# Optimization experiments

Hardware: AMD Instinct MI355X
Metric: run time of the kernel (lower is better)

## Reference

```python
import jax, jax.numpy as jnp
import numpy as np

B, S, DIM = 4, 1024, 2048
HQ, HKV, HD = 16, 4, 128  # query heads, kv heads, head dim
G = HQ // HKV             # GQA group size


def _rope(t, freqs):
    # t: (B, S, H, HD); freqs: (S, HD//2) angles. Llama-style: adjacent pairs
    # (even, odd) treated as (real, imag) and rotated by exp(i*theta).
    tr = t.reshape(t.shape[:-1] + (HD // 2, 2))
    cos = jnp.cos(freqs)[None, :, None, :]
    sin = jnp.sin(freqs)[None, :, None, :]
    re = tr[..., 0] * cos - tr[..., 1] * sin
    im = tr[..., 0] * sin + tr[..., 1] * cos
    return jnp.stack([re, im], axis=-1).reshape(t.shape)


def setup_inputs() -> dict:
    key = jax.random.key(0)
    ks = jax.random.split(key, 5)
    x = jax.random.normal(ks[0], (B, S, DIM), jnp.float32)
    # rotary angles: outer(t, 1/10000^(2i/d))
    inv_freq = 1.0 / (10000.0 ** (np.arange(0, HD, 2, dtype=np.float32) / HD))
    freqs = jnp.asarray(np.outer(np.arange(S, dtype=np.float32), inv_freq))
    # additive causal mask (finite large negative for numerical safety)
    i = jnp.arange(S)
    mask = jnp.where(i[None, :] <= i[:, None], 0.0, -1e9).astype(jnp.float32)
    std = 0.02
    wq = jax.random.normal(ks[1], (HQ * HD, DIM), jnp.float32) * std
    wk = jax.random.normal(ks[2], (HKV * HD, DIM), jnp.float32) * std
    wv = jax.random.normal(ks[3], (HKV * HD, DIM), jnp.float32) * std
    wo = jax.random.normal(ks[4], (DIM, DIM), jnp.float32) * std
    return {"x": x, "start_pos": 0, "freqs": freqs, "mask": mask,
            "wq": wq, "wk": wk, "wv": wv, "wo": wo}


def reference(x, start_pos, freqs, mask, wq, wk, wv, wo):
    b, s, _ = x.shape
    q = (x @ wq.T).reshape(b, s, HQ, HD)
    k = (x @ wk.T).reshape(b, s, HKV, HD)
    v = (x @ wv.T).reshape(b, s, HKV, HD)
    q = _rope(q, freqs)
    k = _rope(k, freqs)
    # GQA: group query heads per kv head, avoiding repeat_kv materialization
    qg = q.reshape(b, s, HKV, G, HD)
    scores = jnp.einsum('bskgd,btkd->bkgst', qg, k) / np.float32(np.sqrt(HD))
    scores = scores + mask  # (S,S) broadcasts over (b, kv, g, s, t)
    p = jax.nn.softmax(scores, axis=-1)
    o = jnp.einsum('bkgst,btkd->bskgd', p, v).reshape(b, s, HQ * HD)
    return o @ wo.T
```

## Files before the change

kernel.cpp:

```cpp
#include <hip/hip_runtime.h>

typedef unsigned short u16;
typedef unsigned int u32;
typedef __bf16 bf16x8 __attribute__((ext_vector_type(8)));
typedef float floatx4 __attribute__((ext_vector_type(4)));

#if __has_builtin(__builtin_amdgcn_exp2f)
#define EXP2F(x) __builtin_amdgcn_exp2f(x)
#else
#define EXP2F(x) __expf((x) * 0.6931471805599453f)
#endif

__device__ __forceinline__ u16 f2bf(float x) {
  union { float f; u32 u; } v; v.f = x;
  u32 r = v.u + 0x7fffu + ((v.u >> 16) & 1u);
  return (u16)(r >> 16);
}
__device__ __forceinline__ float bf2f(u16 x) {
  union { float f; u32 u; } v; v.u = ((u32)x) << 16;
  return v.f;
}

__device__ __forceinline__ void gl_lds16(const u16* g, u16* l) {
  __builtin_amdgcn_global_load_lds((const __attribute__((address_space(1))) void*)g,
                                   (__attribute__((address_space(3))) void*)l, 16, 0, 0);
}

__global__ __launch_bounds__(256) void cvt_all(const float* __restrict__ x,
                                               const float* __restrict__ wq,
                                               const float* __restrict__ wk,
                                               const float* __restrict__ wv,
                                               const float* __restrict__ wo,
                                               u16* __restrict__ xb, u16* __restrict__ wqb,
                                               u16* __restrict__ wkb, u16* __restrict__ wvb,
                                               u16* __restrict__ wob) {
  int i = blockIdx.x * 256 + threadIdx.x;
  const float* s; u16* d; int off;
  if (i < 2097152)      { s = x;  d = xb;  off = 0; }
  else if (i < 3145728) { s = wq; d = wqb; off = 2097152; }
  else if (i < 3407872) { s = wk; d = wkb; off = 3145728; }
  else if (i < 3670016) { s = wv; d = wvb; off = 3407872; }
  else                  { s = wo; d = wob; off = 3670016; }
  i -= off;
  float4 v = ((const float4*)s)[i];
  uint2 o;
  o.x = (u32)f2bf(v.x) | ((u32)f2bf(v.y) << 16);
  o.y = (u32)f2bf(v.z) | ((u32)f2bf(v.w) << 16);
  ((uint2*)d)[i] = o;
}

__global__ __launch_bounds__(256) void rope_both(u16* __restrict__ qb, u16* __restrict__ kb,
                                                 const float* __restrict__ fr) {
  int idx = blockIdx.x * 256 + threadIdx.x;
  u16* t; int lgH; float scale;
  if (idx < 4194304) { t = qb; lgH = 4; scale = 0.08838834764831845f * 1.4426950408889634f; }
  else               { t = kb; lgH = 2; scale = 1.0f; idx -= 4194304; }
  int p = idx & 63;
  int bsh = idx >> 6;
  int s = (bsh >> lgH) & 1023;
  float th = fr[s * 64 + p];
  float sn, cs;
  sincosf(th, &sn, &cs);
  u32* base = (u32*)(t + (size_t)bsh * 128 + p * 2);
  u32 pr = *base;
  float e = bf2f((u16)(pr & 0xffffu));
  float o = bf2f((u16)(pr >> 16));
  u16 re = f2bf((e * cs - o * sn) * scale);
  u16 im = f2bf((e * sn + o * cs) * scale);
  *base = (u32)re | ((u32)im << 16);
}

__device__ __forceinline__ void gemm_core(const u16* __restrict__ A, const u16* __restrict__ Bw,
                                          u16* sA, u16* sB, int m0, int n0,
                                          floatx4 acc[4][4]) {
  const int tid = threadIdx.x;
  const int wave = tid >> 6, lane = tid & 63;
  const int quad = lane >> 4, l16 = lane & 15;
  const int wm = (wave >> 1) * 64, wn = (wave & 1) * 64;
  const int srow = wave * 8 + (lane >> 3);
  const int scol = (((lane & 7) ^ ((lane >> 3) & 7)) * 8);
  const int lds_off = wave * 512 + lane * 8;
  const int swA = (l16 & 7);
  for (int k0 = 0; k0 < 2048; k0 += 64) {
    __syncthreads();
    #pragma unroll
    for (int c = 0; c < 4; c++) {
      gl_lds16(A + (size_t)(m0 + c * 32 + srow) * 2048 + k0 + scol, sA + c * 2048 + lds_off);
      gl_lds16(Bw + (size_t)(n0 + c * 32 + srow) * 2048 + k0 + scol, sB + c * 2048 + lds_off);
    }
    __syncthreads();
    #pragma unroll
    for (int ks = 0; ks < 64; ks += 32) {
      const int pc = ((((ks >> 3) + quad) ^ swA) << 3);
      bf16x8 af[4], bw[4];
      #pragma unroll
      for (int i = 0; i < 4; i++)
        af[i] = *(const bf16x8*)&sA[(wm + i * 16 + l16) * 64 + pc];
      #pragma unroll
      for (int j = 0; j < 4; j++)
        bw[j] = *(const bf16x8*)&sB[(wn + j * 16 + l16) * 64 + pc];
      #pragma unroll
      for (int i = 0; i < 4; i++)
        #pragma unroll
        for (int j = 0; j < 4; j++)
          acc[i][j] = __builtin_amdgcn_mfma_f32_16x16x32_bf16(af[i], bw[j], acc[i][j], 0, 0, 0);
    }
  }
}

__global__ __launch_bounds__(256, 3) void gemm_qkv(const u16* __restrict__ xb,
                                                   const u16* __restrict__ wqb,
                                                   const u16* __restrict__ wkb,
                                                   const u16* __restrict__ wvb,
                                                   u16* __restrict__ qb, u16* __restrict__ kb,
                                                   u16* __restrict__ vtb) {
  __shared__ __align__(16) u16 sA[128 * 64];
  __shared__ __align__(16) u16 sB[128 * 64];
  const int by = blockIdx.y;
  const u16* Bw; int n0, mode;
  if (by < 16)      { Bw = wqb; n0 = by * 128;        mode = 0; }
  else if (by < 20) { Bw = wkb; n0 = (by - 16) * 128; mode = 1; }
  else              { Bw = wvb; n0 = (by - 20) * 128; mode = 2; }
  const int m0 = blockIdx.x * 128;
  floatx4 acc[4][4] = {};
  gemm_core(xb, Bw, sA, sB, m0, n0, acc);
  const int tid = threadIdx.x;
  const int wave = tid >> 6, lane = tid & 63;
  const int quad = lane >> 4, l16 = lane & 15;
  const int wm = (wave >> 1) * 64, wn = (wave & 1) * 64;
  #pragma unroll
  for (int i = 0; i < 4; i++) {
    #pragma unroll
    for (int j = 0; j < 4; j++) {
      const int row0 = m0 + wm + i * 16 + quad * 4;
      const int col = n0 + wn + j * 16 + l16;
      #pragma unroll
      for (int r = 0; r < 4; r++) {
        int m = row0 + r;
        u16 val = f2bf(acc[i][j][r]);
        if (mode == 0) {
          qb[(size_t)m * 2048 + col] = val;
        } else if (mode == 1) {
          kb[(size_t)m * 512 + col] = val;
        } else {
          int b = m >> 10, sI = m & 1023, kvh = col >> 7, hd = col & 127;
          vtb[((size_t)((b * 4 + kvh) * 128 + hd)) * 1024 + sI] = val;
        }
      }
    }
  }
}

__global__ __launch_bounds__(256, 3) void gemm_out(const u16* __restrict__ ob,
                                                   const u16* __restrict__ wob,
                                                   float* __restrict__ Cf) {
  __shared__ __align__(16) u16 sA[128 * 64];
  __shared__ __align__(16) u16 sB[128 * 64];
  const int m0 = blockIdx.x * 128, n0 = blockIdx.y * 128;
  floatx4 acc[4][4] = {};
  gemm_core(ob, wob, sA, sB, m0, n0, acc);
  const int tid = threadIdx.x;
  const int wave = tid >> 6, lane = tid & 63;
  const int quad = lane >> 4, l16 = lane & 15;
  const int wm = (wave >> 1) * 64, wn = (wave & 1) * 64;
  #pragma unroll
  for (int i = 0; i < 4; i++) {
    #pragma unroll
    for (int j = 0; j < 4; j++) {
      const int row0 = m0 + wm + i * 16 + quad * 4;
      const int col = n0 + wn + j * 16 + l16;
      #pragma unroll
      for (int r = 0; r < 4; r++)
        Cf[(size_t)(row0 + r) * 2048 + col] = acc[i][j][r];
    }
  }
}

__device__ __forceinline__ void attn_chunk(const u16* __restrict__ qbaseHead,
                                           const u16* __restrict__ kbase,
                                           const u16* __restrict__ vbase,
                                           int qr0, int kt_begin, int kt_end,
                                           u16* myP, floatx4 (&o_acc)[2][8],
                                           float (&l_part)[2], int quad, int l16) {
  const floatx4 vzero = {0.f, 0.f, 0.f, 0.f};
  #pragma unroll
  for (int i = 0; i < 2; i++) {
    l_part[i] = 0.f;
    #pragma unroll
    for (int j = 0; j < 8; j++) o_acc[i][j] = vzero;
  }
  bf16x8 aq[2][4];
  #pragma unroll
  for (int i = 0; i < 2; i++)
    #pragma unroll
    for (int ks = 0; ks < 4; ks++)
      aq[i][ks] = *(const bf16x8*)(qbaseHead + (size_t)(qr0 + i * 16 + l16) * 2048 + ks * 32 + quad * 8);

  bf16x8 bk[2][4];
  #pragma unroll
  for (int j = 0; j < 4; j++)
    bk[0][j] = *(const bf16x8*)(kbase + (size_t)(kt_begin * 64 + j * 16 + l16) * 512 + quad * 8);

  for (int kt = kt_begin; kt < kt_end; kt++) {
    const int t0 = kt * 64;
    const int t0n = (kt + 1 < kt_end) ? t0 + 64 : t0;
    floatx4 s_acc[4][2];
    #pragma unroll
    for (int j = 0; j < 4; j++)
      #pragma unroll
      for (int i = 0; i < 2; i++) s_acc[j][i] = vzero;
    bf16x8 bv[2][8];
    #pragma unroll
    for (int j2 = 0; j2 < 8; j2++)
      bv[0][j2] = *(const bf16x8*)(vbase + (size_t)(j2 * 16 + l16) * 1024 + t0 + quad * 8);
    #pragma unroll
    for (int ks = 0; ks < 4; ks++) {
      const int nks = (ks + 1) & 3;
      const int nt0 = (ks == 3) ? t0n : t0;
      #pragma unroll
      for (int j = 0; j < 4; j++)
        bk[(ks + 1) & 1][j] =
            *(const bf16x8*)(kbase + (size_t)(nt0 + j * 16 + l16) * 512 + nks * 32 + quad * 8);
      #pragma unroll
      for (int j = 0; j < 4; j++)
        #pragma unroll
        for (int i = 0; i < 2; i++)
          s_acc[j][i] = __builtin_amdgcn_mfma_f32_16x16x32_bf16(bk[ks & 1][j], aq[i][ks], s_acc[j][i], 0, 0, 0);
    }
    #pragma unroll
    for (int j2 = 0; j2 < 8; j2++)
      bv[1][j2] = *(const bf16x8*)(vbase + (size_t)(j2 * 16 + l16) * 1024 + t0 + 32 + quad * 8);
    const bool nomask = (t0 + 63 <= qr0);
    #pragma unroll
    for (int i = 0; i < 2; i++) {
      const int qrow = qr0 + i * 16 + l16;
      #pragma unroll
      for (int j = 0; j < 4; j++) {
        const int key0 = t0 + j * 16 + quad * 4;
        float e0, e1, e2, e3;
        if (nomask) {
          e0 = EXP2F(s_acc[j][i][0]);
          e1 = EXP2F(s_acc[j][i][1]);
          e2 = EXP2F(s_acc[j][i][2]);
          e3 = EXP2F(s_acc[j][i][3]);
        } else {
          e0 = (key0 + 0 <= qrow) ? EXP2F(s_acc[j][i][0]) : 0.f;
          e1 = (key0 + 1 <= qrow) ? EXP2F(s_acc[j][i][1]) : 0.f;
          e2 = (key0 + 2 <= qrow) ? EXP2F(s_acc[j][i][2]) : 0.f;
          e3 = (key0 + 3 <= qrow) ? EXP2F(s_acc[j][i][3]) : 0.f;
        }
        l_part[i] += (e0 + e1) + (e2 + e3);
        uint2 w;
        w.x = (u32)f2bf(e0) | ((u32)f2bf(e1) << 16);
        w.y = (u32)f2bf(e2) | ((u32)f2bf(e3) << 16);
        *(uint2*)&myP[(i * 16 + l16) * 68 + j * 16 + quad * 4] = w;
      }
    }
    #pragma unroll
    for (int ks2 = 0; ks2 < 2; ks2++) {
      bf16x8 ap[2];
      #pragma unroll
      for (int i = 0; i < 2; i++)
        ap[i] = *(const bf16x8*)&myP[(i * 16 + l16) * 68 + ks2 * 32 + quad * 8];
      #pragma unroll
      for (int i = 0; i < 2; i++)
        #pragma unroll
        for (int j2 = 0; j2 < 8; j2++)
          o_acc[i][j2] = __builtin_amdgcn_mfma_f32_16x16x32_bf16(ap[i], bv[ks2][j2], o_acc[i][j2], 0, 0, 0);
    }
  }
}

__device__ __forceinline__ void store_out(u16* __restrict__ obaseHead, int qr0,
                                          floatx4 (&o_acc)[2][8], float (&l_part)[2],
                                          int quad, int l16) {
  #pragma unroll
  for (int i = 0; i < 2; i++) {
    float lr = l_part[i];
    lr += __shfl_xor(lr, 16);
    lr += __shfl_xor(lr, 32);
    #pragma unroll
    for (int r = 0; r < 4; r++) {
      const float inv = 1.f / __shfl(lr, quad * 4 + r);
      const int row = qr0 + i * 16 + quad * 4 + r;
      #pragma unroll
      for (int j = 0; j < 8; j++)
        obaseHead[(size_t)row * 2048 + j * 16 + l16] = f2bf(o_acc[i][j][r] * inv);
    }
  }
}

__global__ __launch_bounds__(128)
__attribute__((amdgpu_waves_per_eu(2, 2)))
void flash_attn(const u16* __restrict__ q,
                const u16* __restrict__ k,
                const u16* __restrict__ vt,
                u16* __restrict__ o) {
  __shared__ __align__(16) char smem[26112];
  const int tid = threadIdx.x;
  const int wave = tid >> 6, lane = tid & 63;
  const int quad = lane >> 4, l16 = lane & 15;
  const int bi = blockIdx.x;
  const int h = bi & 63;
  const int b = h >> 4, hq = h & 15, kv = (hq >> 2);
  const int c = 31 - (bi >> 6);
  const int Tc = (32 * c + 31) / 64 + 1;
  const int tMid = Tc >> 1;
  u16* myP = (u16*)(smem + wave * 4352);
  float* ldsO = (float*)(smem + 8704);
  float* ldsL = (float*)(smem + 8704 + 16896);

  const u16* qbaseHead = q + (size_t)b * 2097152 + hq * 128;
  const u16* kbase = k + (size_t)b * 524288 + kv * 128;
  const u16* vbase = vt + (size_t)(b * 4 + kv) * 131072;
  u16* obaseHead = o + (size_t)b * 2097152 + hq * 128;

  floatx4 o_acc[2][8];
  float l_part[2];
  if (wave == 0) {
    attn_chunk(qbaseHead, kbase, vbase, c * 32, 0, tMid, myP, o_acc, l_part, quad, l16);
    #pragma unroll
    for (int i = 0; i < 2; i++) {
      ldsL[i * 64 + lane] = l_part[i];
      #pragma unroll
      for (int j = 0; j < 8; j++)
        #pragma unroll
        for (int r = 0; r < 4; r++)
          ldsO[(i * 16 + quad * 4 + r) * 132 + j * 16 + l16] = o_acc[i][j][r];
    }
    __syncthreads();
  } else {
    attn_chunk(qbaseHead, kbase, vbase, c * 32, tMid, Tc, myP, o_acc, l_part, quad, l16);
    __syncthreads();
    #pragma unroll
    for (int i = 0; i < 2; i++) {
      l_part[i] += ldsL[i * 64 + lane];
      #pragma unroll
      for (int j = 0; j < 8; j++)
        #pragma unroll
        for (int r = 0; r < 4; r++)
          o_acc[i][j][r] += ldsO[(i * 16 + quad * 4 + r) * 132 + j * 16 + l16];
    }
    store_out(obaseHead, c * 32, o_acc, l_part, quad, l16);
  }
}

extern "C" void kernel_launch(void* const* d_in, const int* in_sizes, int n_in,
                              void* d_out, int out_size, void* d_ws, size_t ws_size,
                              hipStream_t stream) {
  const float* x  = (const float*)d_in[0];
  const float* fr = (const float*)d_in[2];
  const float* wq = (const float*)d_in[4];
  const float* wk = (const float*)d_in[5];
  const float* wv = (const float*)d_in[6];
  const float* wo = (const float*)d_in[7];
  float* out = (float*)d_out;

  char* ws = (char*)d_ws;
  u16* xb  = (u16*)(ws + 0);
  u16* wqb = (u16*)(ws + 16777216);
  u16* wkb = (u16*)(ws + 25165824);
  u16* wvb = (u16*)(ws + 27262976);
  u16* wob = (u16*)(ws + 29360128);
  u16* qb  = (u16*)(ws + 37748736);
  u16* kb  = (u16*)(ws + 54525952);
  u16* vtb = (u16*)(ws + 58720256);
  u16* ob  = (u16*)(ws + 62914560);

  cvt_all<<<18432, 256, 0, stream>>>(x, wq, wk, wv, wo, xb, wqb, wkb, wvb, wob);
  gemm_qkv<<<dim3(32, 24), 256, 0, stream>>>(xb, wqb, wkb, wvb, qb, kb, vtb);
  rope_both<<<20480, 256, 0, stream>>>(qb, kb, fr);
  flash_attn<<<2048, 128, 0, stream>>>(qb, kb, vtb, ob);
  gemm_out<<<dim3(32, 16), 256, 0, stream>>>(ob, wob, out);
}
```

Baseline: 306.9 us.

## Share K/V tiles across GQA heads via swizzled LDS staging in flash attention

Restructures flash attention so each 256-thread block serves two query heads of one KV head over 64 query rows. K tiles (double-buffered) and V tiles are staged into LDS with async global-to-LDS loads and an XOR swizzle, so the four waves reuse one copy instead of each wave loading K/V from global memory. It drops the old split-KV two-wave reduction in favour of a causal-balanced block ordering (pairing short and long rows). The cost is two block-wide barriers per tile and fewer, larger blocks, which may lower occupancy.

```diff
diff --git a/kernel.cpp b/kernel.cpp
--- a/kernel.cpp
+++ b/kernel.cpp
@@ -176,12 +176,60 @@
   }
 }
 
-__device__ __forceinline__ void attn_chunk(const u16* __restrict__ qbaseHead,
-                                           const u16* __restrict__ kbase,
-                                           const u16* __restrict__ vbase,
-                                           int qr0, int kt_begin, int kt_end,
-                                           u16* myP, floatx4 (&o_acc)[2][8],
-                                           float (&l_part)[2], int quad, int l16) {
+__device__ __forceinline__ void store_out(u16* __restrict__ obaseHead, int qr0,
+                                          floatx4 (&o_acc)[2][8], float (&l_part)[2],
+                                          int quad, int l16) {
+  #pragma unroll
+  for (int i = 0; i < 2; i++) {
+    float lr = l_part[i];
+    lr += __shfl_xor(lr, 16);
+    lr += __shfl_xor(lr, 32);
+    #pragma unroll
+    for (int r = 0; r < 4; r++) {
+      const float inv = 1.f / __shfl(lr, quad * 4 + r);
+      const int row = qr0 + i * 16 + quad * 4 + r;
+      #pragma unroll
+      for (int j = 0; j < 8; j++)
+        obaseHead[(size_t)row * 2048 + j * 16 + l16] = f2bf(o_acc[i][j][r] * inv);
+    }
+  }
+}
+
+__global__ __launch_bounds__(256)
+__attribute__((amdgpu_waves_per_eu(2, 2)))
+void flash_attn(const u16* __restrict__ q,
+                const u16* __restrict__ k,
+                const u16* __restrict__ vt,
+                u16* __restrict__ o) {
+  __shared__ __align__(16) u16 sK[2][64 * 128];
+  __shared__ __align__(16) u16 sV[128 * 64];
+  __shared__ __align__(16) u16 sP[4][32 * 64];
+  const int tid = threadIdx.x;
+  const int wave = tid >> 6, lane = tid & 63;
+  const int quad = lane >> 4, l16 = lane & 15;
+  const int bi = blockIdx.x;
+  const int bkv = bi & 15;
+  const int b = bkv >> 2, kv = bkv & 3;
+  const int hp = (bi >> 4) & 1;
+  const int u = bi >> 5;
+  const int m = (u < 8) ? u : 23 - u;
+  const int qh = kv * 4 + hp * 2 + (wave >> 1);
+  const int qr0 = m * 64 + (wave & 1) * 32;
+
+  const u16* qbase = q + (size_t)b * 2097152 + qh * 128;
+  const u16* vbase = vt + (size_t)(b * 4 + kv) * 131072;
+  u16* obase = o + (size_t)b * 2097152 + qh * 128;
+  u16* myP = &sP[wave][0];
+
+  bf16x8 aq[2][4];
+  #pragma unroll
+  for (int i = 0; i < 2; i++)
+    #pragma unroll
+    for (int ks = 0; ks < 4; ks++)
+      aq[i][ks] = *(const bf16x8*)(qbase + (size_t)(qr0 + i * 16 + l16) * 2048 + ks * 32 + quad * 8);
+
+  floatx4 o_acc[2][8];
+  float l_part[2];
   const floatx4 vzero = {0.f, 0.f, 0.f, 0.f};
   #pragma unroll
   for (int i = 0; i < 2; i++) {
@@ -189,54 +237,71 @@
     #pragma unroll
     for (int j = 0; j < 8; j++) o_acc[i][j] = vzero;
   }
-  bf16x8 aq[2][4];
-  #pragma unroll
-  for (int i = 0; i < 2; i++)
-    #pragma unroll
-    for (int ks = 0; ks < 4; ks++)
-      aq[i][ks] = *(const bf16x8*)(qbaseHead + (size_t)(qr0 + i * 16 + l16) * 2048 + ks * 32 + quad * 8);
-
-  bf16x8 bk[2][4];
-  #pragma unroll
-  for (int j = 0; j < 4; j++)
-    bk[0][j] = *(const bf16x8*)(kbase + (size_t)(kt_begin * 64 + j * 16 + l16) * 512 + quad * 8);
-
-  for (int kt = kt_begin; kt < kt_end; kt++) {
-    const int t0 = kt * 64;
-    const int t0n = (kt + 1 < kt_end) ? t0 + 64 : t0;
+
+  #define STAGE_K(T, PAR)                                                         \
+    {                                                                             \
+      const u16* kb_t = k + (size_t)(b * 1024 + (T) * 64) * 512 + kv * 128;       \
+      _Pragma("unroll")                                                           \
+      for (int v = 0; v < 4; v++) {                                               \
+        int ci = v * 256 + tid;                                                   \
+        int r = ci >> 4, c = ci & 15;                                             \
+        gl_lds16(kb_t + r * 512 + ((c ^ (r & 7)) << 3), &sK[PAR][ci * 8]);        \
+      }                                                                           \
+    }
+  #define STAGE_V(T)                                                              \
+    {                                                                             \
+      _Pragma("unroll")                                                           \
+      for (int v = 0; v < 4; v++) {                                               \
+        int ci = v * 256 + tid;                                                   \
+        int r = ci >> 3, c = ci & 7;                                              \
+        gl_lds16(vbase + r * 1024 + (T) * 64 + ((c ^ (r & 7)) << 3), &sV[ci * 8]); \
+      }                                                                           \
+    }
+
+  STAGE_K(0, 0);
+  __syncthreads();
+
+  for (int t = 0; t <= m; t++) {
+    STAGE_V(t);
+    if (t < m) STAGE_K(t + 1, (t + 1) & 1);
+
+    const u16* kcur = &sK[t & 1][0];
     floatx4 s_acc[4][2];
     #pragma unroll
     for (int j = 0; j < 4; j++)
       #pragma unroll
       for (int i = 0; i < 2; i++) s_acc[j][i] = vzero;
-    bf16x8 bv[2][8];
-    #pragma unroll
-    for (int j2 = 0; j2 < 8; j2++)
-      bv[0][j2] = *(const bf16x8*)(vbase + (size_t)(j2 * 16 + l16) * 1024 + t0 + quad * 8);
+    bf16x8 bkA[4], bkB[4];
+    #pragma unroll
+    for (int j = 0; j < 4; j++) {
+      const int R = j * 16 + l16;
+      bkA[j] = *(const bf16x8*)&kcur[R * 128 + ((quad ^ (R & 7)) << 3)];
+    }
     #pragma unroll
     for (int ks = 0; ks < 4; ks++) {
-      const int nks = (ks + 1) & 3;
-      const int nt0 = (ks == 3) ? t0n : t0;
-      #pragma unroll
-      for (int j = 0; j < 4; j++)
-        bk[(ks + 1) & 1][j] =
-            *(const bf16x8*)(kbase + (size_t)(nt0 + j * 16 + l16) * 512 + nks * 32 + quad * 8);
+      bf16x8* cur = (ks & 1) ? bkB : bkA;
+      bf16x8* nxt = (ks & 1) ? bkA : bkB;
+      if (ks < 3) {
+        #pragma unroll
+        for (int j = 0; j < 4; j++) {
+          const int R = j * 16 + l16;
+          nxt[j] = *(const bf16x8*)&kcur[R * 128 + ((((ks + 1) * 4 + quad) ^ (R & 7)) << 3)];
+        }
+      }
       #pragma unroll
       for (int j = 0; j < 4; j++)
         #pragma unroll
         for (int i = 0; i < 2; i++)
-          s_acc[j][i] = __builtin_amdgcn_mfma_f32_16x16x32_bf16(bk[ks & 1][j], aq[i][ks], s_acc[j][i], 0, 0, 0);
-    }
-    #pragma unroll
-    for (int j2 = 0; j2 < 8; j2++)
-      bv[1][j2] = *(const bf16x8*)(vbase + (size_t)(j2 * 16 + l16) * 1024 + t0 + 32 + quad * 8);
-    const bool nomask = (t0 + 63 <= qr0);
+          s_acc[j][i] = __builtin_amdgcn_mfma_f32_16x16x32_bf16(cur[j], aq[i][ks], s_acc[j][i], 0, 0, 0);
+    }
+
+    const bool nomask = (t < m);
     #pragma unroll
     for (int i = 0; i < 2; i++) {
       const int qrow = qr0 + i * 16 + l16;
       #pragma unroll
       for (int j = 0; j < 4; j++) {
-        const int key0 = t0 + j * 16 + quad * 4;
+        const int key0 = t * 64 + j * 16 + quad * 4;
         float e0, e1, e2, e3;
         if (nomask) {
           e0 = EXP2F(s_acc[j][i][0]);
@@ -253,96 +318,39 @@
         uint2 w;
         w.x = (u32)f2bf(e0) | ((u32)f2bf(e1) << 16);
         w.y = (u32)f2bf(e2) | ((u32)f2bf(e3) << 16);
-        *(uint2*)&myP[(i * 16 + l16) * 68 + j * 16 + quad * 4] = w;
-      }
-    }
+        const int ri = i * 16 + l16;
+        *(uint2*)&myP[ri * 64 + (((2 * j + (quad >> 1)) ^ (ri & 7)) << 3) + (quad & 1) * 4] = w;
+      }
+    }
+
+    __syncthreads();
+
     #pragma unroll
     for (int ks2 = 0; ks2 < 2; ks2++) {
-      bf16x8 ap[2];
-      #pragma unroll
-      for (int i = 0; i < 2; i++)
-        ap[i] = *(const bf16x8*)&myP[(i * 16 + l16) * 68 + ks2 * 32 + quad * 8];
+      bf16x8 ap[2], bvf[8];
+      #pragma unroll
+      for (int j2 = 0; j2 < 8; j2++) {
+        const int R = j2 * 16 + l16;
+        bvf[j2] = *(const bf16x8*)&sV[R * 64 + (((ks2 * 4 + quad) ^ (R & 7)) << 3)];
+      }
+      #pragma unroll
+      for (int i = 0; i < 2; i++) {
+        const int ri = i * 16 + l16;
+        ap[i] = *(const bf16x8*)&myP[ri * 64 + (((ks2 * 4 + quad) ^ (ri & 7)) << 3)];
+      }
       #pragma unroll
       for (int i = 0; i < 2; i++)
         #pragma unroll
         for (int j2 = 0; j2 < 8; j2++)
-          o_acc[i][j2] = __builtin_amdgcn_mfma_f32_16x16x32_bf16(ap[i], bv[ks2][j2], o_acc[i][j2], 0, 0, 0);
-    }
-  }
-}
-
-__device__ __forceinline__ void store_out(u16* __restrict__ obaseHead, int qr0,
-                                          floatx4 (&o_acc)[2][8], float (&l_part)[2],
-                                          int quad, int l16) {
-  #pragma unroll
-  for (int i = 0; i < 2; i++) {
-    float lr = l_part[i];
-    lr += __shfl_xor(lr, 16);
-    lr += __shfl_xor(lr, 32);
-    #pragma unroll
-    for (int r = 0; r < 4; r++) {
-      const float inv = 1.f / __shfl(lr, quad * 4 + r);
-      const int row = qr0 + i * 16 + quad * 4 + r;
-      #pragma unroll
-      for (int j = 0; j < 8; j++)
-        obaseHead[(size_t)row * 2048 + j * 16 + l16] = f2bf(o_acc[i][j][r] * inv);
-    }
-  }
-}
-
-__global__ __launch_bounds__(128)
-__attribute__((amdgpu_waves_per_eu(2, 2)))
-void flash_attn(const u16* __restrict__ q,
-                const u16* __restrict__ k,
-                const u16* __restrict__ vt,
-                u16* __restrict__ o) {
-  __shared__ __align__(16) char smem[26112];
-  const int tid = threadIdx.x;
-  const int wave = tid >> 6, lane = tid & 63;
-  const int quad = lane >> 4, l16 = lane & 15;
-  const int bi = blockIdx.x;
-  const int h = bi & 63;
-  const int b = h >> 4, hq = h & 15, kv = (hq >> 2);
-  const int c = 31 - (bi >> 6);
-  const int Tc = (32 * c + 31) / 64 + 1;
-  const int tMid = Tc >> 1;
-  u16* myP = (u16*)(smem + wave * 4352);
-  float* ldsO = (float*)(smem + 8704);
-  float* ldsL = (float*)(smem + 8704 + 16896);
-
-  const u16* qbaseHead = q + (size_t)b * 2097152 + hq * 128;
-  const u16* kbase = k + (size_t)b * 524288 + kv * 128;
-  const u16* vbase = vt + (size_t)(b * 4 + kv) * 131072;
-  u16* obaseHead = o + (size_t)b * 2097152 + hq * 128;
-
-  floatx4 o_acc[2][8];
-  float l_part[2];
-  if (wave == 0) {
-    attn_chunk(qbaseHead, kbase, vbase, c * 32, 0, tMid, myP, o_acc, l_part, quad, l16);
-    #pragma unroll
-    for (int i = 0; i < 2; i++) {
-      ldsL[i * 64 + lane] = l_part[i];
-      #pragma unroll
-      for (int j = 0; j < 8; j++)
-        #pragma unroll
-        for (int r = 0; r < 4; r++)
-          ldsO[(i * 16 + quad * 4 + r) * 132 + j * 16 + l16] = o_acc[i][j][r];
-    }
+          o_acc[i][j2] = __builtin_amdgcn_mfma_f32_16x16x32_bf16(ap[i], bvf[j2], o_acc[i][j2], 0, 0, 0);
+    }
+
     __syncthreads();
-  } else {
-    attn_chunk(qbaseHead, kbase, vbase, c * 32, tMid, Tc, myP, o_acc, l_part, quad, l16);
-    __syncthreads();
-    #pragma unroll
-    for (int i = 0; i < 2; i++) {
-      l_part[i] += ldsL[i * 64 + lane];
-      #pragma unroll
-      for (int j = 0; j < 8; j++)
-        #pragma unroll
-        for (int r = 0; r < 4; r++)
-          o_acc[i][j][r] += ldsO[(i * 16 + quad * 4 + r) * 132 + j * 16 + l16];
-    }
-    store_out(obaseHead, c * 32, o_acc, l_part, quad, l16);
-  }
+  }
+
+  store_out(obase, qr0, o_acc, l_part, quad, l16);
+  #undef STAGE_K
+  #undef STAGE_V
 }
 
 extern "C" void kernel_launch(void* const* d_in, const int* in_sizes, int n_in,
@@ -370,6 +378,6 @@
   cvt_all<<<18432, 256, 0, stream>>>(x, wq, wk, wv, wo, xb, wqb, wkb, wvb, wob);
   gemm_qkv<<<dim3(32, 24), 256, 0, stream>>>(xb, wqb, wkb, wvb, qb, kb, vtb);
   rope_both<<<20480, 256, 0, stream>>>(qb, kb, fr);
-  flash_attn<<<2048, 128, 0, stream>>>(qb, kb, vtb, ob);
+  flash_attn<<<512, 256, 0, stream>>>(qb, kb, vtb, ob);
   gemm_out<<<dim3(32, 16), 256, 0, stream>>>(ob, wob, out);
 }
```

Measured after the change: 267.0 us. 13.0% less time.
